# Kernel optimization log

Measured on AMD Instinct MI355X. Metric: run time of the kernel, lower is better.

The kernel has to match this reference:

```python
import jax, jax.numpy as jnp
import numpy as np

N = 100000          # total nodes
E = 3200000         # total edges (avg degree 32)
B = 100             # num graphs
NPG = N // B        # nodes per graph (uniform -> to_dense_batch is a reshape)
D_IN, D_H, D_E, N_CLS = 128, 64, 32, 10


def setup_inputs() -> dict:
    key = jax.random.key(0)
    ks = jax.random.split(key, 12)
    x = jax.random.normal(ks[0], (N, D_IN), jnp.float32)
    # edges strictly within each graph: offset by graph block
    epg = E // B
    offs = (jnp.arange(E, dtype=jnp.int32) // epg) * NPG
    src = jax.random.randint(ks[1], (E,), 0, NPG, jnp.int32) + offs
    dst = jax.random.randint(ks[2], (E,), 0, NPG, jnp.int32) + offs
    edge_index = jnp.stack([src, dst])
    batch = jnp.repeat(jnp.arange(B, dtype=jnp.int32), NPG)

    def glorot(k, fi, fo):
        return jax.random.normal(k, (fi, fo), jnp.float32) * (1.0 / np.sqrt(fi))

    return {
        "x": x, "edge_index": edge_index, "batch": batch,
        "W_a1": glorot(ks[3], D_IN, D_H), "b_a1": jnp.zeros((D_H,), jnp.float32),
        "W_a2": glorot(ks[4], D_H, D_E),  "b_a2": jnp.zeros((D_E,), jnp.float32),
        "W_x1": glorot(ks[5], D_IN, D_H), "b_x1": jnp.zeros((D_H,), jnp.float32),
        "W_x2": glorot(ks[6], D_H, D_E),  "b_x2": jnp.zeros((D_E,), jnp.float32),
        "W_lin": glorot(ks[7], D_E * D_E, N_CLS),
        "b_lin": jnp.zeros((N_CLS,), jnp.float32),
    }


def _gcn(x, W, b, src, dst, n):
    """PyG GCNConv(improved=True): sym-norm with self-loop weight 2."""
    h = x @ W                                                   # [n, out]
    deg = jax.ops.segment_sum(jnp.ones_like(dst, h.dtype), dst, n) + 2.0
    dinv = jax.lax.rsqrt(deg)                                   # [n]
    coef = dinv[src] * dinv[dst]                                # [E]
    agg = jax.ops.segment_sum(h[src] * coef[:, None], dst, n)   # gather-scatter
    agg = agg + (2.0 * dinv * dinv)[:, None] * h                # self-loop term
    return agg + b


def _segment_softmax(v, seg, nseg):
    m = jax.ops.segment_max(v, seg, nseg)
    e = jnp.exp(v - m[seg])
    s = jax.ops.segment_sum(e, seg, nseg)
    return e / s[seg]


def reference(x, edge_index, batch, W_a1, b_a1, W_a2, b_a2,
              W_x1, b_x1, W_x2, b_x2, W_lin, b_lin):
    src, dst = edge_index[0], edge_index[1]
    n = x.shape[0]
    a1 = jax.nn.relu(_gcn(x, W_a1, b_a1, src, dst, n))
    a2 = _segment_softmax(_gcn(a1, W_a2, b_a2, src, dst, n), batch, B)
    x1 = jax.nn.relu(_gcn(x, W_x1, b_x1, src, dst, n))
    x2 = jax.nn.relu(_gcn(x1, W_x2, b_x2, src, dst, n))
    # uniform graph sizes -> to_dense_batch is a reshape (no padding needed)
    a_b = a2.reshape(B, NPG, D_E)
    x_b = x2.reshape(B, NPG, D_E)
    prods = jnp.einsum('bne,bnf->bef', a_b, x_b)   # bmm(a^T, x): [B, D_E, D_E]
    flat = prods.reshape(B, D_E * D_E)
    return jax.nn.softmax(flat @ W_lin + b_lin, axis=-1)
```

## Files before the change

kernel.cpp:

```cpp
#include <hip/hip_runtime.h>
#include <hip/hip_bf16.h>
#include <hip/hip_fp16.h>

#define N_NODES 100000
#define N_EDGES 3200000
#define NB      100
#define NPG     1000
#define EPG     32000
#define DIN     128
#define DH      64
#define DE      32
#define NCLS    10



__global__ __launch_bounds__(1024) void k_sort(const int* __restrict__ src,
                                               const int* __restrict__ dst,
                                               int* __restrict__ rowptr,
                                               float* __restrict__ dinv,
                                               unsigned int* __restrict__ esrc) {
    __shared__ __align__(16) unsigned short buf[EPG];
    __shared__ int cnt[NPG];
    __shared__ int pre[NPG];
    __shared__ int sm[1024];
    __shared__ unsigned short dh[NPG];
    int g = (blockIdx.x & 7) + 8 * (blockIdx.x >> 3);
    if (g >= NB) return;
    int t = threadIdx.x;
    int ebase = g * EPG, nbase = g * NPG;
    if (t < NPG) cnt[t] = 0;
    __syncthreads();
    for (int i = t; i < EPG; i += 1024)
        atomicAdd(&cnt[dst[ebase + i] - nbase], 1);
    __syncthreads();
    int v = (t < NPG) ? cnt[t] : 0;
    if (t < NPG) {
        float dv = rsqrtf((float)v + 2.0f);
        dinv[nbase + t] = dv;
        dh[t] = __half_as_ushort(__float2half_rn(dv));
    }
    sm[t] = v;
    __syncthreads();
    for (int off = 1; off < 1024; off <<= 1) {
        int x = (t >= off) ? sm[t - off] : 0;
        __syncthreads();
        sm[t] += x;
        __syncthreads();
    }
    if (t < NPG) {
        int ex = sm[t] - v;
        pre[t] = ex;
        rowptr[nbase + t] = ebase + ex;
    }
    if (g == NB - 1 && t == 0) rowptr[N_NODES] = N_EDGES;
    __syncthreads();
    for (int i = t; i < EPG; i += 1024) {
        int e = ebase + i;
        int d = dst[e] - nbase;
        int s = src[e] - nbase;
        int pos = atomicAdd(&pre[d], 1);
        buf[pos] = (unsigned short)s;
    }
    __syncthreads();
    uint4* gout = (uint4*)(esrc + ebase);
    const ushort4* lbuf = (const ushort4*)buf;
    for (int i = t; i < EPG / 4; i += 1024) {
        ushort4 s4 = lbuf[i];
        uint4 o;
        o.x = s4.x | ((unsigned)dh[s4.x] << 16);
        o.y = s4.y | ((unsigned)dh[s4.y] << 16);
        o.z = s4.z | ((unsigned)dh[s4.z] << 16);
        o.w = s4.w | ((unsigned)dh[s4.w] << 16);
        gout[i] = o;
    }
}


__global__ __launch_bounds__(256) void k_gemm1(const float* __restrict__ x,
                                               const float* __restrict__ Wa,
                                               const float* __restrict__ Wx,
                                               unsigned short* __restrict__ h16) {
    __shared__ float xs[32][128];
    __shared__ float ws[32][128];
    int xcd = blockIdx.x & 7, slot = blockIdx.x >> 3;
    int g = xcd + 8 * (slot >> 5);
    int chunk = slot & 31;
    if (g >= NB) return;
    int row0 = g * NPG + chunk * 32;
    int t = threadIdx.x;
    for (int i = 0; i < 4; i++) {
        int idx = t + 256 * i;
        int r = idx >> 5, k4 = idx & 31;
        int rr = row0 + r; if (rr >= N_NODES) rr = N_NODES - 1;
        *(float4*)&xs[r][k4 * 4] = *(const float4*)&x[(size_t)rr * 128 + k4 * 4];
    }
    float acc[4][4] = {};
    int rg = t >> 5, cg = t & 31;
    for (int kt = 0; kt < 4; kt++) {
        __syncthreads();
        for (int i = 0; i < 4; i++) {
            int idx = t + 256 * i;
            int kk = idx >> 5, c4 = idx & 31;
            int k = kt * 32 + kk, c = c4 * 4;
            float4 v;
            if (c < 64) v = *(const float4*)&Wa[k * 64 + c];
            else        v = *(const float4*)&Wx[k * 64 + (c - 64)];
            *(float4*)&ws[kk][c] = v;
        }
        __syncthreads();
        for (int kk = 0; kk < 32; kk++) {
            float4 w = *(float4*)&ws[kk][cg * 4];
            float xv[4];
            for (int i = 0; i < 4; i++) xv[i] = xs[rg * 4 + i][kt * 32 + kk];
            for (int i = 0; i < 4; i++) {
                acc[i][0] += xv[i] * w.x; acc[i][1] += xv[i] * w.y;
                acc[i][2] += xv[i] * w.z; acc[i][3] += xv[i] * w.w;
            }
        }
    }
    for (int i = 0; i < 4; i++) {
        int r = row0 + rg * 4 + i;
        if (r < N_NODES) {
            union { ushort4 u; __half2 h[2]; } pk;
            pk.h[0] = __floats2half2_rn(acc[i][0], acc[i][1]);
            pk.h[1] = __floats2half2_rn(acc[i][2], acc[i][3]);
            *(ushort4*)&h16[r * 128 + cg * 4] = pk.u;
        }
    }
}


__global__ __launch_bounds__(256) void k_agg128(const unsigned short* __restrict__ h16,
                                                const int* __restrict__ rowptr,
                                                const unsigned int* __restrict__ esrc,
                                                const float* __restrict__ dinv,
                                                const float* __restrict__ ba,
                                                const float* __restrict__ bx,
                                                unsigned short* __restrict__ outB16) {
    int xcd = blockIdx.x & 7, slot = blockIdx.x >> 3;
    int gi = slot / 250, chunk = slot - gi * 250;
    int g = xcd + 8 * gi;
    if (g >= NB) return;
    int nl   = chunk * 4 + (threadIdx.x >> 6);
    int wid  = g * NPG + nl;
    int lane = threadIdx.x & 63;
    int sub = lane >> 4;
    int cl8 = (lane & 15) * 8;
    const unsigned short* hg = h16 + g * NPG * 128;
    float acc[8] = {};
    union U8 { uint4 u; __half h[8]; };
    int e0 = rowptr[wid], e1 = rowptr[wid + 1];
    int e = e0;
    for (; e + 16 <= e1; e += 16) {
        unsigned pv[4]; U8 r[4];
        #pragma unroll
        for (int j = 0; j < 4; j++) pv[j] = esrc[e + 4 * j + sub];
        #pragma unroll
        for (int j = 0; j < 4; j++) r[j].u = *(const uint4*)&hg[(pv[j] & 0xffffu) * 128 + cl8];
        #pragma unroll
        for (int j = 0; j < 4; j++) {
            float dv = __half2float(__ushort_as_half((unsigned short)(pv[j] >> 16)));
            #pragma unroll
            for (int k = 0; k < 8; k++)
                acc[k] += dv * __half2float(r[j].h[k]);
        }
    }
    for (; e + 8 <= e1; e += 8) {
        #pragma unroll
        for (int j = 0; j < 2; j++) {
            unsigned pv = esrc[e + 4 * j + sub];
            U8 r; r.u = *(const uint4*)&hg[(pv & 0xffffu) * 128 + cl8];
            float dv = __half2float(__ushort_as_half((unsigned short)(pv >> 16)));
            #pragma unroll
            for (int k = 0; k < 8; k++)
                acc[k] += dv * __half2float(r.h[k]);
        }
    }
    for (; e < e1; e += 4) {
        int ee = e + sub;
        unsigned pv; float scale;
        if (ee < e1) { pv = esrc[ee]; scale = 1.0f; }
        else         { pv = esrc[e];  scale = 0.0f; }
        U8 r; r.u = *(const uint4*)&hg[(pv & 0xffffu) * 128 + cl8];
        float dv = scale * __half2float(__ushort_as_half((unsigned short)(pv >> 16)));
        #pragma unroll
        for (int k = 0; k < 8; k++)
            acc[k] += dv * __half2float(r.h[k]);
    }
    #pragma unroll
    for (int k = 0; k < 8; k++) {
        acc[k] += __shfl_xor(acc[k], 16);
        acc[k] += __shfl_xor(acc[k], 32);
    }
    if (sub == 0) {
        float di = dinv[wid];
        float sw = 2.0f * di * di;
        U8 hv; hv.u = *(const uint4*)&hg[nl * 128 + cl8];
        const float* bb = (cl8 < 64) ? &ba[cl8] : &bx[cl8 - 64];
        union { ushort4 u[2]; __half2 h[4]; uint4 q; } pk;
        #pragma unroll
        for (int k = 0; k < 4; k++) {
            float ox = fmaxf(di * acc[2 * k]     + sw * __half2float(hv.h[2 * k])     + bb[2 * k],     0.0f);
            float oy = fmaxf(di * acc[2 * k + 1] + sw * __half2float(hv.h[2 * k + 1]) + bb[2 * k + 1], 0.0f);
            pk.h[k] = __floats2half2_rn(ox, oy);
        }
        *(uint4*)&outB16[wid * 128 + cl8] = pk.q;
    }
}


__global__ __launch_bounds__(256) void k_agg64(const unsigned short* __restrict__ g16,
                                               const int* __restrict__ rowptr,
                                               const unsigned int* __restrict__ esrc,
                                               const float* __restrict__ dinv,
                                               const float* __restrict__ ba2,
                                               const float* __restrict__ bx2,
                                               float* __restrict__ s2) {
    int xcd = blockIdx.x & 7, slot = blockIdx.x >> 3;
    int gi = slot / 250, chunk = slot - gi * 250;
    int g = xcd + 8 * gi;
    if (g >= NB) return;
    int nl   = chunk * 4 + (threadIdx.x >> 6);
    int wid  = g * NPG + nl;
    int lane = threadIdx.x & 63;
    int sub = lane >> 3;
    int cl8 = (lane & 7) * 8;
    const unsigned short* hg = g16 + g * NPG * 64;
    float acc[8] = {};
    union U8 { uint4 u; __half h[8]; };
    int e0 = rowptr[wid], e1 = rowptr[wid + 1];
    int e = e0;
    for (; e + 16 <= e1; e += 16) {
        unsigned pv[2]; U8 r[2];
        #pragma unroll
        for (int j = 0; j < 2; j++) pv[j] = esrc[e + 8 * j + sub];
        #pragma unroll
        for (int j = 0; j < 2; j++) r[j].u = *(const uint4*)&hg[(pv[j] & 0xffffu) * 64 + cl8];
        #pragma unroll
        for (int j = 0; j < 2; j++) {
            float dv = __half2float(__ushort_as_half((unsigned short)(pv[j] >> 16)));
            #pragma unroll
            for (int k = 0; k < 8; k++)
                acc[k] += dv * __half2float(r[j].h[k]);
        }
    }
    for (; e < e1; e += 8) {
        int ee = e + sub;
        unsigned pv; float scale;
        if (ee < e1) { pv = esrc[ee]; scale = 1.0f; }
        else         { pv = esrc[e];  scale = 0.0f; }
        U8 r; r.u = *(const uint4*)&hg[(pv & 0xffffu) * 64 + cl8];
        float dv = scale * __half2float(__ushort_as_half((unsigned short)(pv >> 16)));
        #pragma unroll
        for (int k = 0; k < 8; k++)
            acc[k] += dv * __half2float(r.h[k]);
    }
    #pragma unroll
    for (int k = 0; k < 8; k++) {
        acc[k] += __shfl_xor(acc[k], 8);
        acc[k] += __shfl_xor(acc[k], 16);
        acc[k] += __shfl_xor(acc[k], 32);
    }
    if (sub == 0) {
        float di = dinv[wid];
        float sw = 2.0f * di * di;
        U8 hv; hv.u = *(const uint4*)&hg[nl * 64 + cl8];
        float o[8];
        #pragma unroll
        for (int k = 0; k < 8; k++)
            o[k] = di * acc[k] + sw * __half2float(hv.h[k]);
        if (cl8 < 32) {
            #pragma unroll
            for (int k = 0; k < 8; k++) o[k] += ba2[cl8 + k];
        } else {
            #pragma unroll
            for (int k = 0; k < 8; k++) o[k] = fmaxf(o[k] + bx2[cl8 - 32 + k], 0.0f);
        }
        *(float4*)&s2[wid * 64 + cl8]     = make_float4(o[0], o[1], o[2], o[3]);
        *(float4*)&s2[wid * 64 + cl8 + 4] = make_float4(o[4], o[5], o[6], o[7]);
    }
}


__global__ __launch_bounds__(256) void k_gemm2(const unsigned short* __restrict__ Bm16,
                                               const float* __restrict__ Wa2,
                                               const float* __restrict__ Wx2,
                                               unsigned short* __restrict__ g16) {
    __shared__ float xs[64][132];
    __shared__ float ws[64][68];
    int xcd = blockIdx.x & 7, slot = blockIdx.x >> 3;
    int g = xcd + 8 * (slot >> 4);
    int chunk = slot & 15;
    if (g >= NB) return;
    int row0 = g * NPG + chunk * 64;
    int t = threadIdx.x;
    for (int i = 0; i < 4; i++) {
        int idx = t + 256 * i;
        int k = idx >> 4, c4 = idx & 15, c = c4 * 4;
        float4 v;
        if (c < 32) v = *(const float4*)&Wa2[k * 32 + c];
        else        v = *(const float4*)&Wx2[k * 32 + (c - 32)];
        *(float4*)&ws[k][c] = v;
    }
    for (int i = 0; i < 4; i++) {
        int idx = t + 256 * i;
        int r = idx >> 4, c8 = idx & 15;
        int rr = row0 + r; if (rr >= N_NODES) rr = N_NODES - 1;
        union { uint4 u; __half2 h[4]; } pk;
        pk.u = *(const uint4*)&Bm16[rr * 128 + c8 * 8];
        float2 f0 = __half22float2(pk.h[0]);
        float2 f1 = __half22float2(pk.h[1]);
        float2 f2 = __half22float2(pk.h[2]);
        float2 f3 = __half22float2(pk.h[3]);
        int cb = c8 * 8;
        *(float4*)&xs[r][cb]     = make_float4(f0.x, f0.y, f1.x, f1.y);
        *(float4*)&xs[r][cb + 4] = make_float4(f2.x, f2.y, f3.x, f3.y);
    }
    __syncthreads();
    int cg = t & 15, rg = t >> 4;
    int koff = (cg < 8) ? 0 : 64;
    float acc[4][4] = {};
    for (int k = 0; k < 64; k++) {
        float4 w = *(float4*)&ws[k][cg * 4];
        float xv[4];
        for (int i = 0; i < 4; i++) xv[i] = xs[rg * 4 + i][koff + k];
        for (int i = 0; i < 4; i++) {
            acc[i][0] += xv[i] * w.x; acc[i][1] += xv[i] * w.y;
            acc[i][2] += xv[i] * w.z; acc[i][3] += xv[i] * w.w;
        }
    }
    for (int i = 0; i < 4; i++) {
        int r = row0 + rg * 4 + i;
        if (r < N_NODES) {
            union { ushort4 u; __half2 h[2]; } pk;
            pk.h[0] = __floats2half2_rn(acc[i][0], acc[i][1]);
            pk.h[1] = __floats2half2_rn(acc[i][2], acc[i][3]);
            *(ushort4*)&g16[r * 64 + cg * 4] = pk.u;
        }
    }
}


__global__ __launch_bounds__(512) void k_smax(const float* __restrict__ s2,
                                              float* __restrict__ gmax,
                                              float* __restrict__ sinv) {
    __shared__ float red[16][32];
    int g = (blockIdx.x & 7) + 8 * (blockIdx.x >> 3);
    if (g >= NB) return;
    int t = threadIdx.x;
    int c = t & 31, sub = t >> 5;
    size_t base = (size_t)g * NPG;
    float m = -1e30f;
    for (int n = sub; n < NPG; n += 16)
        m = fmaxf(m, s2[(base + n) * 64 + c]);
    red[sub][c] = m; __syncthreads();
    if (sub == 0) {
        for (int j = 1; j < 16; j++) m = fmaxf(m, red[j][c]);
        red[0][c] = m;
        gmax[g * 32 + c] = m;
    }
    __syncthreads();
    m = red[0][c];
    __syncthreads();
    float sum = 0.0f;
    for (int n = sub; n < NPG; n += 16)
        sum += __expf(s2[(base + n) * 64 + c] - m);
    red[sub][c] = sum; __syncthreads();
    if (sub == 0) {
        for (int j = 1; j < 16; j++) sum += red[j][c];
        sinv[g * 32 + c] = 1.0f / sum;
    }
}


__global__ __launch_bounds__(256) void k_pool(const float* __restrict__ s2,
                                              const float* __restrict__ gmax,
                                              float* __restrict__ prods) {
    __shared__ float ta[25][32];
    __shared__ float tx[25][32];
    __shared__ float gm[32];
    int xcd = blockIdx.x & 7, slot = blockIdx.x >> 3;
    int g = xcd + 8 * (slot >> 3);
    int ch = slot & 7;
    if (g >= NB) return;
    int t = threadIdx.x;
    if (t < 32) gm[t] = gmax[g * 32 + t];
    int e  = t >> 3;
    int f4 = t & 7;
    float a0 = 0.f, a1 = 0.f, a2 = 0.f, a3 = 0.f;
    int base = g * NPG + ch * 125;
    for (int n0 = 0; n0 < 125; n0 += 25) {
        __syncthreads();
        for (int i = t; i < 25 * 16; i += 256) {
            int r = i >> 4, c4 = i & 15;
            float4 v = *(const float4*)&s2[(size_t)(base + n0 + r) * 64 + c4 * 4];
            if (c4 < 8) {
                int cb = c4 * 4;
                v.x = __expf(v.x - gm[cb + 0]);
                v.y = __expf(v.y - gm[cb + 1]);
                v.z = __expf(v.z - gm[cb + 2]);
                v.w = __expf(v.w - gm[cb + 3]);
                *(float4*)&ta[r][cb] = v;
            } else {
                *(float4*)&tx[r][(c4 - 8) * 4] = v;
            }
        }
        __syncthreads();
        #pragma unroll 5
        for (int n = 0; n < 25; n++) {
            float a   = ta[n][e];
            float4 xv = *(float4*)&tx[n][f4 * 4];
            a0 += a * xv.x; a1 += a * xv.y; a2 += a * xv.z; a3 += a * xv.w;
        }
    }
    *(float4*)&prods[((size_t)(g * 8 + ch)) * 1024 + e * 32 + f4 * 4] =
        make_float4(a0, a1, a2, a3);
}


__global__ __launch_bounds__(256) void k_head(const float* __restrict__ prods,
                                              const float* __restrict__ sinv,
                                              const float* __restrict__ Wlin,
                                              const float* __restrict__ blin,
                                              float* __restrict__ out) {
    __shared__ float red[4][NCLS];
    int g = (blockIdx.x & 7) + 8 * (blockIdx.x >> 3);
    if (g >= NB) return;
    int t = threadIdx.x;
    float p[NCLS];
    for (int c = 0; c < NCLS; c++) p[c] = 0.0f;
    const float* pg = &prods[(size_t)g * 8 * 1024];
    for (int j = 0; j < 4; j++) {
        int k = t * 4 + j;
        int e = k >> 5;
        float v = 0.0f;
        #pragma unroll
        for (int q = 0; q < 8; q++) v += pg[q * 1024 + k];
        v *= sinv[g * 32 + e];
        const float* wrow = &Wlin[k * NCLS];
        for (int c = 0; c < NCLS; c++) p[c] += v * wrow[c];
    }
    for (int off = 32; off > 0; off >>= 1)
        for (int c = 0; c < NCLS; c++) p[c] += __shfl_down(p[c], off, 64);
    int wave = t >> 6, lane = t & 63;
    if (lane == 0)
        for (int c = 0; c < NCLS; c++) red[wave][c] = p[c];
    __syncthreads();
    if (t == 0) {
        float logits[NCLS]; float mx = -1e30f;
        for (int c = 0; c < NCLS; c++) {
            logits[c] = red[0][c] + red[1][c] + red[2][c] + red[3][c] + blin[c];
            mx = fmaxf(mx, logits[c]);
        }
        float s = 0.0f;
        for (int c = 0; c < NCLS; c++) { logits[c] = expf(logits[c] - mx); s += logits[c]; }
        float inv = 1.0f / s;
        for (int c = 0; c < NCLS; c++) out[g * NCLS + c] = logits[c] * inv;
    }
}


extern "C" void kernel_launch(void* const* d_in, const int* in_sizes, int n_in,
                              void* d_out, int out_size, void* d_ws, size_t ws_size,
                              hipStream_t stream) {
    const float* x    = (const float*)d_in[0];
    const int*   ei   = (const int*)d_in[1];
    const float* Wa1  = (const float*)d_in[3];
    const float* ba1  = (const float*)d_in[4];
    const float* Wa2  = (const float*)d_in[5];
    const float* ba2  = (const float*)d_in[6];
    const float* Wx1  = (const float*)d_in[7];
    const float* bx1  = (const float*)d_in[8];
    const float* Wx2  = (const float*)d_in[9];
    const float* bx2  = (const float*)d_in[10];
    const float* Wlin = (const float*)d_in[11];
    const float* blin = (const float*)d_in[12];
    float* out = (float*)d_out;

    char* w = (char*)d_ws;
    auto alloc = [&](size_t bytes) -> void* {
        void* p = (void*)w;
        w += (bytes + 255) & ~(size_t)255;
        return p;
    };
    int*            rowptr = (int*)alloc((N_NODES + 1) * sizeof(int));
    float*          dinv   = (float*)alloc(N_NODES * sizeof(float));
    unsigned int*   esrc   = (unsigned int*)alloc((size_t)N_EDGES * sizeof(unsigned int));
    float*          gmax   = (float*)alloc(NB * DE * sizeof(float));
    float*          sinv   = (float*)alloc(NB * DE * sizeof(float));
    float*          prods  = (float*)alloc((size_t)NB * 8 * 1024 * sizeof(float));
    unsigned short* h16    = (unsigned short*)alloc((size_t)N_NODES * 128 * sizeof(unsigned short));
    unsigned short* b16    = (unsigned short*)alloc((size_t)N_NODES * 128 * sizeof(unsigned short));
    unsigned short* g16    = (unsigned short*)alloc((size_t)N_NODES * 64 * sizeof(unsigned short));
    float*          s2     = (float*)alloc((size_t)N_NODES * 64 * sizeof(float));

    const int* srcp = ei;
    const int* dstp = ei + N_EDGES;

    k_sort<<<8 * 13, 1024, 0, stream>>>(srcp, dstp, rowptr, dinv, esrc);
    k_gemm1<<<8 * 13 * 32, 256, 0, stream>>>(x, Wa1, Wx1, h16);
    k_agg128<<<8 * 13 * 250, 256, 0, stream>>>(h16, rowptr, esrc, dinv, ba1, bx1, b16);
    k_gemm2<<<8 * 13 * 16, 256, 0, stream>>>(b16, Wa2, Wx2, g16);
    k_agg64<<<8 * 13 * 250, 256, 0, stream>>>(g16, rowptr, esrc, dinv, ba2, bx2, s2);
    k_smax<<<8 * 13, 512, 0, stream>>>(s2, gmax, sinv);
    k_pool<<<8 * 13 * 8, 256, 0, stream>>>(s2, gmax, prods);
    k_head<<<8 * 13, 256, 0, stream>>>(prods, sinv, Wlin, blin, out);
}
```

Measured before the change: 349.4 us.

## Merge edge sort and first GEMM into one launch, prescale edge source indices

```diff
diff --git a/kernel.cpp b/kernel.cpp
--- a/kernel.cpp
+++ b/kernel.cpp
@@ -11,120 +11,130 @@
 #define DH      64
 #define DE      32
 #define NCLS    10
-
-
-
-__global__ __launch_bounds__(1024) void k_sort(const int* __restrict__ src,
-                                               const int* __restrict__ dst,
-                                               int* __restrict__ rowptr,
-                                               float* __restrict__ dinv,
-                                               unsigned int* __restrict__ esrc) {
-    __shared__ __align__(16) unsigned short buf[EPG];
-    __shared__ int cnt[NPG];
-    __shared__ int pre[NPG];
-    __shared__ int sm[1024];
-    __shared__ unsigned short dh[NPG];
-    int g = (blockIdx.x & 7) + 8 * (blockIdx.x >> 3);
-    if (g >= NB) return;
+#define SORT_BLOCKS 104
+
+
+
+union SharedU {
+    struct {
+        __align__(16) unsigned short buf[EPG];
+        int cnt[NPG];
+        int pre[NPG];
+        int sm[1024];
+        unsigned short dh[NPG];
+    } so;
+    struct {
+        float xs[4][32][128];
+        float ws[32][128];
+    } ge;
+};
+
+__global__ __launch_bounds__(1024) void k_sg(const int* __restrict__ src,
+                                             const int* __restrict__ dst,
+                                             const float* __restrict__ x,
+                                             const float* __restrict__ Wa,
+                                             const float* __restrict__ Wx,
+                                             int* __restrict__ rowptr,
+                                             float* __restrict__ dinv,
+                                             unsigned int* __restrict__ esrc,
+                                             unsigned short* __restrict__ h16) {
+    __shared__ SharedU S;
     int t = threadIdx.x;
-    int ebase = g * EPG, nbase = g * NPG;
-    if (t < NPG) cnt[t] = 0;
-    __syncthreads();
-    for (int i = t; i < EPG; i += 1024)
-        atomicAdd(&cnt[dst[ebase + i] - nbase], 1);
-    __syncthreads();
-    int v = (t < NPG) ? cnt[t] : 0;
-    if (t < NPG) {
-        float dv = rsqrtf((float)v + 2.0f);
-        dinv[nbase + t] = dv;
-        dh[t] = __half_as_ushort(__float2half_rn(dv));
-    }
-    sm[t] = v;
-    __syncthreads();
-    for (int off = 1; off < 1024; off <<= 1) {
-        int x = (t >= off) ? sm[t - off] : 0;
-        __syncthreads();
-        sm[t] += x;
-        __syncthreads();
-    }
-    if (t < NPG) {
-        int ex = sm[t] - v;
-        pre[t] = ex;
-        rowptr[nbase + t] = ebase + ex;
-    }
-    if (g == NB - 1 && t == 0) rowptr[N_NODES] = N_EDGES;
-    __syncthreads();
-    for (int i = t; i < EPG; i += 1024) {
-        int e = ebase + i;
-        int d = dst[e] - nbase;
-        int s = src[e] - nbase;
-        int pos = atomicAdd(&pre[d], 1);
-        buf[pos] = (unsigned short)s;
-    }
-    __syncthreads();
-    uint4* gout = (uint4*)(esrc + ebase);
-    const ushort4* lbuf = (const ushort4*)buf;
-    for (int i = t; i < EPG / 4; i += 1024) {
-        ushort4 s4 = lbuf[i];
-        uint4 o;
-        o.x = s4.x | ((unsigned)dh[s4.x] << 16);
-        o.y = s4.y | ((unsigned)dh[s4.y] << 16);
-        o.z = s4.z | ((unsigned)dh[s4.z] << 16);
-        o.w = s4.w | ((unsigned)dh[s4.w] << 16);
-        gout[i] = o;
-    }
-}
-
-
-__global__ __launch_bounds__(256) void k_gemm1(const float* __restrict__ x,
-                                               const float* __restrict__ Wa,
-                                               const float* __restrict__ Wx,
-                                               unsigned short* __restrict__ h16) {
-    __shared__ float xs[32][128];
-    __shared__ float ws[32][128];
-    int xcd = blockIdx.x & 7, slot = blockIdx.x >> 3;
-    int g = xcd + 8 * (slot >> 5);
-    int chunk = slot & 31;
-    if (g >= NB) return;
-    int row0 = g * NPG + chunk * 32;
-    int t = threadIdx.x;
-    for (int i = 0; i < 4; i++) {
-        int idx = t + 256 * i;
-        int r = idx >> 5, k4 = idx & 31;
-        int rr = row0 + r; if (rr >= N_NODES) rr = N_NODES - 1;
-        *(float4*)&xs[r][k4 * 4] = *(const float4*)&x[(size_t)rr * 128 + k4 * 4];
-    }
-    float acc[4][4] = {};
-    int rg = t >> 5, cg = t & 31;
-    for (int kt = 0; kt < 4; kt++) {
-        __syncthreads();
+    if (blockIdx.x < SORT_BLOCKS) {
+        int g = (blockIdx.x & 7) + 8 * (blockIdx.x >> 3);
+        if (g >= NB) return;
+        int ebase = g * EPG, nbase = g * NPG;
+        if (t < NPG) S.so.cnt[t] = 0;
+        __syncthreads();
+        for (int i = t; i < EPG; i += 1024)
+            atomicAdd(&S.so.cnt[dst[ebase + i] - nbase], 1);
+        __syncthreads();
+        int v = (t < NPG) ? S.so.cnt[t] : 0;
+        if (t < NPG) {
+            float dv = rsqrtf((float)v + 2.0f);
+            dinv[nbase + t] = dv;
+            S.so.dh[t] = __half_as_ushort(__float2half_rn(dv));
+        }
+        S.so.sm[t] = v;
+        __syncthreads();
+        for (int off = 1; off < 1024; off <<= 1) {
+            int xx = (t >= off) ? S.so.sm[t - off] : 0;
+            __syncthreads();
+            S.so.sm[t] += xx;
+            __syncthreads();
+        }
+        if (t < NPG) {
+            int ex = S.so.sm[t] - v;
+            S.so.pre[t] = ex;
+            rowptr[nbase + t] = ebase + ex;
+        }
+        if (g == NB - 1 && t == 0) rowptr[N_NODES] = N_EDGES;
+        __syncthreads();
+        for (int i = t; i < EPG; i += 1024) {
+            int e = ebase + i;
+            int d = dst[e] - nbase;
+            int s = src[e] - nbase;
+            int pos = atomicAdd(&S.so.pre[d], 1);
+            S.so.buf[pos] = (unsigned short)s;
+        }
+        __syncthreads();
+        uint4* gout = (uint4*)(esrc + ebase);
+        const ushort4* lbuf = (const ushort4*)S.so.buf;
+        for (int i = t; i < EPG / 4; i += 1024) {
+            ushort4 s4 = lbuf[i];
+            uint4 o;
+            o.x = ((unsigned)s4.x * 16) | ((unsigned)S.so.dh[s4.x] << 16);
+            o.y = ((unsigned)s4.y * 16) | ((unsigned)S.so.dh[s4.y] << 16);
+            o.z = ((unsigned)s4.z * 16) | ((unsigned)S.so.dh[s4.z] << 16);
+            o.w = ((unsigned)s4.w * 16) | ((unsigned)S.so.dh[s4.w] << 16);
+            gout[i] = o;
+        }
+    } else {
+        int b = blockIdx.x - SORT_BLOCKS;
+        int xcd = b & 7, slot = b >> 3;
+        int g = xcd + 8 * (slot >> 3);
+        int chunk = slot & 7;
+        if (g >= NB) return;
+        int q  = t >> 8;
+        int tq = t & 255;
+        int row0 = g * NPG + chunk * 128 + q * 32;
         for (int i = 0; i < 4; i++) {
-            int idx = t + 256 * i;
-            int kk = idx >> 5, c4 = idx & 31;
-            int k = kt * 32 + kk, c = c4 * 4;
-            float4 v;
-            if (c < 64) v = *(const float4*)&Wa[k * 64 + c];
-            else        v = *(const float4*)&Wx[k * 64 + (c - 64)];
-            *(float4*)&ws[kk][c] = v;
-        }
-        __syncthreads();
-        for (int kk = 0; kk < 32; kk++) {
-            float4 w = *(float4*)&ws[kk][cg * 4];
-            float xv[4];
-            for (int i = 0; i < 4; i++) xv[i] = xs[rg * 4 + i][kt * 32 + kk];
-            for (int i = 0; i < 4; i++) {
-                acc[i][0] += xv[i] * w.x; acc[i][1] += xv[i] * w.y;
-                acc[i][2] += xv[i] * w.z; acc[i][3] += xv[i] * w.w;
+            int idx = tq + 256 * i;
+            int r = idx >> 5, k4 = idx & 31;
+            int rr = row0 + r; if (rr >= N_NODES) rr = N_NODES - 1;
+            *(float4*)&S.ge.xs[q][r][k4 * 4] = *(const float4*)&x[(size_t)rr * 128 + k4 * 4];
+        }
+        float acc[4][4] = {};
+        int rg = tq >> 5, cg = tq & 31;
+        for (int kt = 0; kt < 4; kt++) {
+            __syncthreads();
+            {
+                int kk = t >> 5, c4 = t & 31;
+                int k = kt * 32 + kk, c = c4 * 4;
+                float4 v;
+                if (c < 64) v = *(const float4*)&Wa[k * 64 + c];
+                else        v = *(const float4*)&Wx[k * 64 + (c - 64)];
+                *(float4*)&S.ge.ws[kk][c] = v;
             }
-        }
-    }
-    for (int i = 0; i < 4; i++) {
-        int r = row0 + rg * 4 + i;
-        if (r < N_NODES) {
-            union { ushort4 u; __half2 h[2]; } pk;
-            pk.h[0] = __floats2half2_rn(acc[i][0], acc[i][1]);
-            pk.h[1] = __floats2half2_rn(acc[i][2], acc[i][3]);
-            *(ushort4*)&h16[r * 128 + cg * 4] = pk.u;
+            __syncthreads();
+            for (int kk = 0; kk < 32; kk++) {
+                float4 w = *(float4*)&S.ge.ws[kk][cg * 4];
+                float xv[4];
+                for (int i = 0; i < 4; i++) xv[i] = S.ge.xs[q][rg * 4 + i][kt * 32 + kk];
+                for (int i = 0; i < 4; i++) {
+                    acc[i][0] += xv[i] * w.x; acc[i][1] += xv[i] * w.y;
+                    acc[i][2] += xv[i] * w.z; acc[i][3] += xv[i] * w.w;
+                }
+            }
+        }
+        for (int i = 0; i < 4; i++) {
+            int r = row0 + rg * 4 + i;
+            if (r < N_NODES) {
+                union { ushort4 u; __half2 h[2]; } pk;
+                pk.h[0] = __floats2half2_rn(acc[i][0], acc[i][1]);
+                pk.h[1] = __floats2half2_rn(acc[i][2], acc[i][3]);
+                *(ushort4*)&h16[r * 128 + cg * 4] = pk.u;
+            }
         }
     }
 }
@@ -145,8 +155,8 @@
     int wid  = g * NPG + nl;
     int lane = threadIdx.x & 63;
     int sub = lane >> 4;
-    int cl8 = (lane & 15) * 8;
-    const unsigned short* hg = h16 + g * NPG * 128;
+    int cl  = lane & 15;
+    const uint4* hg4 = (const uint4*)(h16 + g * NPG * 128);
     float acc[8] = {};
     union U8 { uint4 u; __half h[8]; };
     int e0 = rowptr[wid], e1 = rowptr[wid + 1];
@@ -156,7 +166,7 @@
         #pragma unroll
         for (int j = 0; j < 4; j++) pv[j] = esrc[e + 4 * j + sub];
         #pragma unroll
-        for (int j = 0; j < 4; j++) r[j].u = *(const uint4*)&hg[(pv[j] & 0xffffu) * 128 + cl8];
+        for (int j = 0; j < 4; j++) r[j].u = hg4[(pv[j] & 0xffffu) + cl];
         #pragma unroll
         for (int j = 0; j < 4; j++) {
             float dv = __half2float(__ushort_as_half((unsigned short)(pv[j] >> 16)));
@@ -169,7 +179,7 @@
         #pragma unroll
         for (int j = 0; j < 2; j++) {
             unsigned pv = esrc[e + 4 * j + sub];
-            U8 r; r.u = *(const uint4*)&hg[(pv & 0xffffu) * 128 + cl8];
+            U8 r; r.u = hg4[(pv & 0xffffu) + cl];
             float dv = __half2float(__ushort_as_half((unsigned short)(pv >> 16)));
             #pragma unroll
             for (int k = 0; k < 8; k++)
@@ -181,7 +191,7 @@
         unsigned pv; float scale;
         if (ee < e1) { pv = esrc[ee]; scale = 1.0f; }
         else         { pv = esrc[e];  scale = 0.0f; }
-        U8 r; r.u = *(const uint4*)&hg[(pv & 0xffffu) * 128 + cl8];
+        U8 r; r.u = hg4[(pv & 0xffffu) + cl];
         float dv = scale * __half2float(__ushort_as_half((unsigned short)(pv >> 16)));
         #pragma unroll
         for (int k = 0; k < 8; k++)
@@ -195,9 +205,10 @@
     if (sub == 0) {
         float di = dinv[wid];
         float sw = 2.0f * di * di;
-        U8 hv; hv.u = *(const uint4*)&hg[nl * 128 + cl8];
+        U8 hv; hv.u = hg4[nl * 16 + cl];
+        int cl8 = cl * 8;
         const float* bb = (cl8 < 64) ? &ba[cl8] : &bx[cl8 - 64];
-        union { ushort4 u[2]; __half2 h[4]; uint4 q; } pk;
+        union { __half2 h[4]; uint4 q; } pk;
         #pragma unroll
         for (int k = 0; k < 4; k++) {
             float ox = fmaxf(di * acc[2 * k]     + sw * __half2float(hv.h[2 * k])     + bb[2 * k],     0.0f);
@@ -224,8 +235,8 @@
     int wid  = g * NPG + nl;
     int lane = threadIdx.x & 63;
     int sub = lane >> 3;
-    int cl8 = (lane & 7) * 8;
-    const unsigned short* hg = g16 + g * NPG * 64;
+    int cl  = lane & 7;
+    const uint4* gg4 = (const uint4*)(g16 + g * NPG * 64);
     float acc[8] = {};
     union U8 { uint4 u; __half h[8]; };
     int e0 = rowptr[wid], e1 = rowptr[wid + 1];
@@ -235,7 +246,7 @@
         #pragma unroll
         for (int j = 0; j < 2; j++) pv[j] = esrc[e + 8 * j + sub];
         #pragma unroll
-        for (int j = 0; j < 2; j++) r[j].u = *(const uint4*)&hg[(pv[j] & 0xffffu) * 64 + cl8];
+        for (int j = 0; j < 2; j++) r[j].u = gg4[((pv[j] & 0xffffu) >> 1) + cl];
         #pragma unroll
         for (int j = 0; j < 2; j++) {
             float dv = __half2float(__ushort_as_half((unsigned short)(pv[j] >> 16)));
@@ -249,7 +260,7 @@
         unsigned pv; float scale;
         if (ee < e1) { pv = esrc[ee]; scale = 1.0f; }
         else         { pv = esrc[e];  scale = 0.0f; }
-        U8 r; r.u = *(const uint4*)&hg[(pv & 0xffffu) * 64 + cl8];
+        U8 r; r.u = gg4[((pv & 0xffffu) >> 1) + cl];
         float dv = scale * __half2float(__ushort_as_half((unsigned short)(pv >> 16)));
         #pragma unroll
         for (int k = 0; k < 8; k++)
@@ -264,7 +275,8 @@
     if (sub == 0) {
         float di = dinv[wid];
         float sw = 2.0f * di * di;
-        U8 hv; hv.u = *(const uint4*)&hg[nl * 64 + cl8];
+        U8 hv; hv.u = gg4[nl * 8 + cl];
+        int cl8 = cl * 8;
         float o[8];
         #pragma unroll
         for (int k = 0; k < 8; k++)
@@ -497,8 +509,8 @@
     const int* srcp = ei;
     const int* dstp = ei + N_EDGES;
 
-    k_sort<<<8 * 13, 1024, 0, stream>>>(srcp, dstp, rowptr, dinv, esrc);
-    k_gemm1<<<8 * 13 * 32, 256, 0, stream>>>(x, Wa1, Wx1, h16);
+    k_sg<<<SORT_BLOCKS + 8 * 13 * 8, 1024, 0, stream>>>(srcp, dstp, x, Wa1, Wx1,
+                                                        rowptr, dinv, esrc, h16);
     k_agg128<<<8 * 13 * 250, 256, 0, stream>>>(h16, rowptr, esrc, dinv, ba1, bx1, b16);
     k_gemm2<<<8 * 13 * 16, 256, 0, stream>>>(b16, Wa2, Wx2, g16);
     k_agg64<<<8 * 13 * 250, 256, 0, stream>>>(g16, rowptr, esrc, dinv, ba2, bx2, s2);
```

Measured after the change: 312.9 us. 10.5% less time.
